# Kernel optimization log

Hardware: AMD Instinct MI355X
Metric: run time of the kernel (lower is better)

Reference implementation:

```python
import jax, jax.numpy as jnp
import numpy as np

EPS = 1e-6


def smooth(p):
    # smooth_distribution: clamp Bernoulli params away from {0,1}
    return jnp.clip(p, EPS, 1.0 - EPS)


def bern_logprob(p, x):
    # Bernoulli(p).log_prob(x) = x*log(p) + (1-x)*log(1-p)
    return x * jnp.log(p) + (1.0 - x) * jnp.log1p(-p)


def binary_row_reduce(A, b, k):
    # GF(2) Gaussian elimination on [A | b]; A:(k,n) binary float, b:(k,)
    M = jnp.concatenate([A, b[:, None]], axis=1)  # (k, n+1)
    rows = jnp.arange(k)
    for i in range(k):  # k is a small static int (25)
        col = M[:, i]
        cand = jnp.where((rows >= i) & (col > 0.5), rows, k)
        p = jnp.minimum(jnp.min(cand), k - 1)  # pivot row (fallback k-1 if none; prob ~0 for random A)
        ri, rp = M[i], M[p]
        M = M.at[i].set(rp)
        M = M.at[p].set(ri)
        elim = (M[:, i] > 0.5) & (rows != i)
        M = jnp.where(elim[:, None], jnp.mod(M + M[i], 2.0), M)
    return M[:, :-1], M[:, -1]


def compute_term1(logq, logp):
    # stable [sum_s q*log p]/[sum_s q], summed over batch; logq,logp: (S,B)
    m = jnp.max(logq, axis=0)                                  # (B,)
    w = jnp.exp(logq - m)                                      # (S,B)
    neg_num = m + jnp.log(jnp.sum(w * (-logp), axis=0))
    pos_den = m + jnp.log(jnp.sum(w, axis=0))
    return -jnp.sum(jnp.exp(neg_num - pos_den))


def setup_inputs() -> dict:
    key = jax.random.key(0)
    ks = jax.random.split(key, 5)
    nx, nz, B = 2048, 256, 512
    wr = float(np.sqrt(6.0 / (nx + nz)))
    xr = float(np.sqrt(6.0 / nx))
    zr = float(np.sqrt(6.0 / nz))
    U = jax.random.uniform(ks[0], (nz, nx), minval=-wr, maxval=wr)
    V = jax.random.uniform(ks[1], (nx, nz), minval=-wr, maxval=wr)
    x_bias = jax.random.uniform(ks[2], (nx,), minval=-xr, maxval=xr)
    z_bias = jax.random.uniform(ks[3], (nz,), minval=-zr, maxval=zr)
    xin = (jax.random.uniform(ks[4], (B, nx)) < 0.5).astype(jnp.float32)
    return {"xin": xin, "U": U, "V": V, "x_bias": x_bias, "z_bias": z_bias,
            "S": 10, "k": 25, "T": 30}


def reference(xin, U, V, x_bias, z_bias, S, k, T):
    dt = xin.dtype
    key = jax.random.key(42)
    kz, kx, kA, kb = jax.random.split(key, 4)

    # q(z|x) and samples  -------------------------------------------------
    q = smooth(jax.nn.sigmoid(xin @ U.T + z_bias))                     # (B, nz)
    samples_z = (jax.random.uniform(kz, (S,) + q.shape) < q).astype(dt)  # (S,B,nz)
    ps = smooth(jax.nn.sigmoid(jnp.einsum('sbz,xz->sbx', samples_z, V) + x_bias))  # (S,B,nx)
    xouts = (jax.random.uniform(kx, ps.shape) < ps).astype(dt)

    # projected ELBO over T random GF(2) hash constraints ------------------
    nz = U.shape[0]
    A_all = (jax.random.uniform(kA, (T, k, nz)) < 0.5).astype(dt)
    b_all = (jax.random.uniform(kb, (T, k)) < 0.5).astype(dt)
    pz = smooth(jax.nn.sigmoid(z_bias))                                # (nz,)

    def elbo_t(carry, Ab):
        A, b = Ab
        C, bp = binary_row_reduce(A, b, k)                             # (k,nz),(k,)
        proj = jnp.mod(jnp.einsum('sbz,kz->sbk', samples_z[:, :, k:], C[:, k:]) + bp, 2.0)
        sz = samples_z.at[:, :, :k].set(proj)                          # (S,B,nz)
        logq_zi = bern_logprob(q, sz).sum(axis=2)                      # (S,B)
        logp_z = bern_logprob(pz, sz).sum(axis=2)                      # (S,B)
        ps_t = smooth(jax.nn.sigmoid(jnp.einsum('sbz,xz->sbx', sz, V) + x_bias))
        logp_x = bern_logprob(ps_t, xin).sum(axis=2)                   # (S,B)
        logp = logp_z + logp_x
        term2 = compute_term1(logq_zi, logq_zi)
        term1 = compute_term1(logq_zi, logp)
        return carry, term1 - term2

    _, pelbos = jax.lax.scan(elbo_t, 0.0, (A_all, b_all))
    loss = -jnp.mean(pelbos)
    return q, samples_z, ps, xouts, loss
```

## Files before the change

### kernel.cpp

```cpp
#include <hip/hip_runtime.h>
#include <cstdint>

#define NX 2048
#define NZ 256
#define NB 512
#define NS 10
#define NK 25
#define NT 30
#define SBTOT (NS * NB)

#define LOG2E 1.4426950408889634f
#define LN2 0.6931471805599453f

#define OFF_Q 0
#define OFF_SAMP (NB * NZ)
#define OFF_PS (OFF_SAMP + SBTOT * NZ)
#define OFF_XO (OFF_PS + SBTOT * NX)
#define OFF_LOSS (OFF_XO + SBTOT * NX)

typedef unsigned long long ull;
typedef __bf16 bf16x8 __attribute__((ext_vector_type(8)));
typedef float f32x4 __attribute__((ext_vector_type(4)));

__host__ __device__ inline void tf2x32(uint32_t k0, uint32_t k1, uint32_t x0, uint32_t x1,
                                       uint32_t& o0, uint32_t& o1) {
  uint32_t k2 = k0 ^ k1 ^ 0x1BD11BDAu;
  x0 += k0; x1 += k1;
#define TF_R(r) { x0 += x1; x1 = (x1 << (r)) | (x1 >> (32 - (r))); x1 ^= x0; }
  TF_R(13) TF_R(15) TF_R(26) TF_R(6)
  x0 += k1; x1 += k2 + 1u;
  TF_R(17) TF_R(29) TF_R(16) TF_R(24)
  x0 += k2; x1 += k0 + 2u;
  TF_R(13) TF_R(15) TF_R(26) TF_R(6)
  x0 += k0; x1 += k1 + 3u;
  TF_R(17) TF_R(29) TF_R(16) TF_R(24)
  x0 += k1; x1 += k2 + 4u;
  TF_R(13) TF_R(15) TF_R(26) TF_R(6)
  x0 += k2; x1 += k0 + 5u;
#undef TF_R
  o0 = x0; o1 = x1;
}

__device__ inline uint32_t tf_select(uint32_t k0, uint32_t k1, uint32_t i, uint32_t h) {
  bool lo = i < h;
  uint32_t x0 = lo ? i : i - h;
  uint32_t x1 = lo ? i + h : i;
  uint32_t o0, o1;
  tf2x32(k0, k1, x0, x1, o0, o1);
  return lo ? o0 : o1;
}

__device__ inline float tf_uniform(uint32_t k0, uint32_t k1, uint32_t i, uint32_t h) {
  uint32_t r = tf_select(k0, k1, i, h);
  return __uint_as_float(0x3f800000u | (r >> 9)) - 1.0f;
}

__device__ inline float sigclip(float a) {
  float p = 1.0f / (1.0f + __expf(-a));
  return fminf(fmaxf(p, 1e-6f), 1.0f - 1e-6f);
}

__device__ inline ushort f2bf(float f) {
  uint32_t u = __float_as_uint(f);
  return (ushort)((u + 0x7FFFu + ((u >> 16) & 1u)) >> 16);
}

__device__ inline float blockReduceSum256(float v, volatile float* s4) {
#pragma unroll
  for (int o = 32; o > 0; o >>= 1) v += __shfl_down(v, o);
  __syncthreads();
  if ((threadIdx.x & 63) == 0) s4[threadIdx.x >> 6] = v;
  __syncthreads();
  return s4[0] + s4[1] + s4[2] + s4[3];
}

__global__ __launch_bounds__(256) void kP0_prep(const float* __restrict__ V,
                                                const float* __restrict__ U,
                                                const float* __restrict__ xin,
                                                const float* __restrict__ z_bias,
                                                ushort* __restrict__ Vbf,
                                                ushort* __restrict__ Vkpad2,
                                                ushort* __restrict__ Uhi,
                                                ushort* __restrict__ Ulo,
                                                ushort* __restrict__ xinbf,
                                                float* __restrict__ baseq,
                                                float* __restrict__ d_lpz,
                                                float* __restrict__ basepz) {
  __shared__ float red[4];
  int e = blockIdx.x * 256 + threadIdx.x;
  {
    int x = e >> 8, k = e & 255;
    float v = V[e];
    Vbf[e] = f2bf(v);
    if (k < 32) Vkpad2[x * 32 + k] = (k < NK) ? f2bf(v * LOG2E) : (ushort)0;
  }
  {
    float u = U[e];
    ushort hi = f2bf(u);
    Uhi[e] = hi;
    float hv = __uint_as_float((uint32_t)hi << 16);
    Ulo[e] = f2bf(u - hv);
  }
  {
    xinbf[e] = (xin[e] > 0.5f) ? (ushort)0x3F80 : (ushort)0;
    int e2 = e + NX * NZ;
    xinbf[e2] = (xin[e2] > 0.5f) ? (ushort)0x3F80 : (ushort)0;
  }
  if (e < NB) baseq[e] = 0.0f;
  if (blockIdx.x == 0) {
    int z = threadIdx.x;
    float pz = sigclip(z_bias[z]);
    float lp = __logf(pz), l1 = __logf(1.0f - pz);
    d_lpz[z] = lp - l1;
    float s = blockReduceSum256(l1, red);
    if (z == 0) *basepz = s;
  }
}

__global__ __launch_bounds__(256) void kW_signdot(const float* __restrict__ xin,
                                                  const ushort* __restrict__ Vkpad2,
                                                  float* __restrict__ W) {
  __shared__ float wred[4][NK];
  int b = blockIdx.x;
  int tid = threadIdx.x;
  float acc[NK];
#pragma unroll
  for (int j = 0; j < NK; ++j) acc[j] = 0.0f;
#pragma unroll
  for (int i = 0; i < 8; ++i) {
    int x = i * 256 + tid;
    float s = 1.0f - 2.0f * xin[(size_t)b * NX + x];
    const uint4* vp = (const uint4*)(Vkpad2 + (size_t)x * 32);
    uint4 q0 = vp[0], q1 = vp[1], q2 = vp[2], q3 = vp[3];
    uint32_t w[16] = {q0.x, q0.y, q0.z, q0.w, q1.x, q1.y, q1.z, q1.w,
                      q2.x, q2.y, q2.z, q2.w, q3.x, q3.y, q3.z, q3.w};
#pragma unroll
    for (int j = 0; j < NK; ++j) {
      uint32_t wd = w[j >> 1];
      float v = __uint_as_float((j & 1) ? (wd & 0xFFFF0000u) : (wd << 16));
      acc[j] = fmaf(s, v, acc[j]);
    }
  }
#pragma unroll
  for (int j = 0; j < NK; ++j) {
#pragma unroll
    for (int o = 1; o < 64; o <<= 1) acc[j] += __shfl_xor(acc[j], o);
  }
  if ((tid & 63) == 0) {
#pragma unroll
    for (int j = 0; j < NK; ++j) wred[tid >> 6][j] = acc[j];
  }
  __syncthreads();
  if (tid < NK) W[b * 32 + tid] = wred[0][tid] + wred[1][tid] + wred[2][tid] + wred[3][tid];
}

__global__ __launch_bounds__(256) void k1a_mfma(const ushort* __restrict__ xinbf,
                                                const ushort* __restrict__ Uhi,
                                                const ushort* __restrict__ Ulo,
                                                const float* __restrict__ z_bias,
                                                float* __restrict__ outq,
                                                float* __restrict__ d_lq,
                                                float* __restrict__ baseq) {
  __shared__ float red[4][16][17];
  int tid = threadIdx.x;
  int wave = tid >> 6, lane = tid & 63, grp = lane >> 4, col = lane & 15;
  int b0 = (blockIdx.x >> 4) * 16;
  int z0 = (blockIdx.x & 15) * 16;
  f32x4 acc = {0.f, 0.f, 0.f, 0.f};
  const ushort* arow = xinbf + (size_t)(b0 + col) * NX + wave * 512 + grp * 8;
  const ushort* bhr = Uhi + (size_t)(z0 + col) * NX + wave * 512 + grp * 8;
  const ushort* blr = Ulo + (size_t)(z0 + col) * NX + wave * 512 + grp * 8;
#pragma unroll 4
  for (int s = 0; s < 16; ++s) {
    bf16x8 a = *(const bf16x8*)(arow + s * 32);
    bf16x8 bh = *(const bf16x8*)(bhr + s * 32);
    bf16x8 bl = *(const bf16x8*)(blr + s * 32);
    acc = __builtin_amdgcn_mfma_f32_16x16x32_bf16(a, bh, acc, 0, 0, 0);
    acc = __builtin_amdgcn_mfma_f32_16x16x32_bf16(a, bl, acc, 0, 0, 0);
  }
#pragma unroll
  for (int r = 0; r < 4; ++r) red[wave][grp * 4 + r][col] = acc[r];
  __syncthreads();
  int bi = tid >> 4, zi = tid & 15;
  float aa = red[0][bi][zi] + red[1][bi][zi] + red[2][bi][zi] + red[3][bi][zi] + z_bias[z0 + zi];
  int b = b0 + bi, z = z0 + zi;
  float q = sigclip(aa);
  outq[b * NZ + z] = q;
  float lq = __logf(q), l1 = __logf(1.0f - q);
  d_lq[b * NZ + z] = lq - l1;
  float s1 = l1;
#pragma unroll
  for (int o = 1; o < 16; o <<= 1) s1 += __shfl_xor(s1, o);
  if (zi == 0) atomicAdd(&baseq[b], s1);
}

__global__ __launch_bounds__(256) void k2_samples(const float* __restrict__ q,
                                                  const float* __restrict__ d_lq,
                                                  const float* __restrict__ d_lpz,
                                                  const ull* __restrict__ Ct,
                                                  const uint32_t* __restrict__ bpmask,
                                                  const float* __restrict__ W,
                                                  float* __restrict__ samp_out,
                                                  ushort* __restrict__ samp16,
                                                  ull* __restrict__ Spack,
                                                  float* __restrict__ qtail,
                                                  float* __restrict__ ptail,
                                                  uint32_t* __restrict__ projb,
                                                  float* __restrict__ Syd,
                                                  uint32_t kz0, uint32_t kz1) {
  __shared__ float red[4];
  __shared__ ull sp_sh[4];
  int sb = blockIdx.x;
  int z = threadIdx.x;
  int b = sb & (NB - 1);
  uint32_t i = (uint32_t)sb * NZ + z;
  const uint32_t h = (uint32_t)SBTOT * NZ / 2;
  float u = tf_uniform(kz0, kz1, i, h);
  float qv = q[b * NZ + z];
  int smp = (u < qv) ? 1 : 0;
  samp_out[i] = (float)smp;
  samp16[i] = smp ? (ushort)0x3F80 : (ushort)0;
  ull m = __ballot(smp);
  if ((z & 63) == 0) { Spack[sb * 4 + (z >> 6)] = m; sp_sh[z >> 6] = m; }
  float dq = (z >= NK && smp) ? d_lq[b * NZ + z] : 0.0f;
  float dp = (z >= NK && smp) ? d_lpz[z] : 0.0f;
  float sq = blockReduceSum256(dq, red);
  float sp = blockReduceSum256(dp, red);
  if (z == 0) { qtail[sb] = sq; ptail[sb] = sp; }
  if (z < 32) {
    int t = z;
    ull s0 = sp_sh[0], s1 = sp_sh[1], s2 = sp_sh[2], s3 = sp_sh[3];
    uint32_t s25 = (uint32_t)(s0 & 0x1FFFFFFull);
    const float* Wb = W + (size_t)b * 32;
    uint32_t out;
    float syd = 0.0f;
    if (t < NT) {
      uint32_t bp = bpmask[t];
      uint32_t pb = 0;
#pragma unroll
      for (int j = 0; j < NK; ++j) {
        const ull* C = Ct + (size_t)(t * NK + j) * 4;
        int par = __popcll(s0 & C[0]) + __popcll(s1 & C[1]) + __popcll(s2 & C[2]) + __popcll(s3 & C[3]);
        uint32_t bit = ((uint32_t)(par ^ (int)(bp >> j))) & 1u;
        pb |= bit << j;
        int d = (int)bit - (int)((s25 >> j) & 1u);
        syd = fmaf((float)d, Wb[j], syd);
      }
      out = pb;
    } else {
      out = s25;
    }
    projb[sb * 32 + t] = out;
    Syd[sb * 32 + t] = syd;
  }
}

__global__ __launch_bounds__(256) void k3m_gemm(const ushort* __restrict__ samp16,
                                                const ushort* __restrict__ Vbf,
                                                const float* __restrict__ x_bias,
                                                ushort* __restrict__ base2,
                                                float* __restrict__ ps_out,
                                                float* __restrict__ xo_out,
                                                uint32_t kx0, uint32_t kx1) {
  __shared__ __align__(16) char smem[2 * 2112 * 4];
  ushort* As = (ushort*)smem;
  ushort* Bs = (ushort*)(smem + 8192);
  float* Tt = (float*)smem;

  int tid = threadIdx.x;
  int wave = tid >> 6, lane = tid & 63, grp = lane >> 4, col = lane & 15;
  int x0 = blockIdx.x * 128;
  int sb0 = blockIdx.y * 32;
  f32x4 acc[2][4];
#pragma unroll
  for (int mi = 0; mi < 2; ++mi)
#pragma unroll
    for (int ni = 0; ni < 4; ++ni) acc[mi][ni] = (f32x4){0.f, 0.f, 0.f, 0.f};

  for (int k0 = 0; k0 < NZ; k0 += 32) {
    {
      int rowb = tid >> 2, kcb = (tid & 3) << 3;
      int sbrow = (rowb < 32) ? (sb0 + rowb) : (sb0 + 2528 + rowb);
      *(uint4*)&Bs[rowb * 32 + kcb] = *(const uint4*)&samp16[(size_t)sbrow * NZ + k0 + kcb];
#pragma unroll
      for (int c = tid; c < 512; c += 256) {
        int rowa = c >> 2, kca = (c & 3) << 3;
        *(uint4*)&As[rowa * 32 + kca] = *(const uint4*)&Vbf[(size_t)(x0 + rowa) * NZ + k0 + kca];
      }
    }
    __syncthreads();
    bf16x8 af[2], bfv[4];
#pragma unroll
    for (int mi = 0; mi < 2; ++mi)
      af[mi] = *(const bf16x8*)&As[(wave * 32 + mi * 16 + col) * 32 + grp * 8];
#pragma unroll
    for (int ni = 0; ni < 4; ++ni)
      bfv[ni] = *(const bf16x8*)&Bs[(ni * 16 + col) * 32 + grp * 8];
#pragma unroll
    for (int mi = 0; mi < 2; ++mi)
#pragma unroll
      for (int ni = 0; ni < 4; ++ni)
        acc[mi][ni] = __builtin_amdgcn_mfma_f32_16x16x32_bf16(af[mi], bfv[ni], acc[mi][ni], 0, 0, 0);
    __syncthreads();
  }

  const uint32_t HH = (uint32_t)(SBTOT / 2) * (uint32_t)NX;
#pragma unroll
  for (int pi = 0; pi < 2; ++pi) {
    __syncthreads();
#pragma unroll
    for (int mi = 0; mi < 2; ++mi) {
      int cbase = wave * 32 + mi * 16 + grp * 4;
      *(float4*)&Tt[col * 132 + cbase] = *(float4*)&acc[mi][pi];
      *(float4*)&Tt[2112 + col * 132 + cbase] = *(float4*)&acc[mi][pi + 2];
    }
    __syncthreads();
#pragma unroll
    for (int pass = 0; pass < 2; ++pass) {
      int r = pass * 8 + (tid >> 5);
      int c = (tid & 31) * 4;
      float4 t0 = *(float4*)&Tt[r * 132 + c];
      float4 t1 = *(float4*)&Tt[2112 + r * 132 + c];
      float4 xb4 = *(const float4*)(x_bias + x0 + c);
      int sb_a = sb0 + pi * 16 + r;
      size_t off_a = (size_t)sb_a * NX + x0 + c;
      size_t off_b = off_a + (size_t)HH;
      float a0 = t0.x + xb4.x, a1 = t0.y + xb4.y, a2 = t0.z + xb4.z, a3 = t0.w + xb4.w;
      float b0 = t1.x + xb4.x, b1 = t1.y + xb4.y, b2 = t1.z + xb4.z, b3 = t1.w + xb4.w;
      uint2 bpa, bpb;
      bpa.x = (uint32_t)f2bf(a0 * LOG2E) | ((uint32_t)f2bf(a1 * LOG2E) << 16);
      bpa.y = (uint32_t)f2bf(a2 * LOG2E) | ((uint32_t)f2bf(a3 * LOG2E) << 16);
      bpb.x = (uint32_t)f2bf(b0 * LOG2E) | ((uint32_t)f2bf(b1 * LOG2E) << 16);
      bpb.y = (uint32_t)f2bf(b2 * LOG2E) | ((uint32_t)f2bf(b3 * LOG2E) << 16);
      *(uint2*)(base2 + off_a) = bpa;
      *(uint2*)(base2 + off_b) = bpb;
      float4 pva = make_float4(sigclip(a0), sigclip(a1), sigclip(a2), sigclip(a3));
      float4 pvb = make_float4(sigclip(b0), sigclip(b1), sigclip(b2), sigclip(b3));
      *(float4*)(ps_out + off_a) = pva;
      *(float4*)(ps_out + off_b) = pvb;
      uint32_t fi = (uint32_t)off_a;
      uint32_t r0, r1;
      float4 xva, xvb;
      tf2x32(kx0, kx1, fi + 0u, fi + 0u + HH, r0, r1);
      xva.x = ((__uint_as_float(0x3f800000u | (r0 >> 9)) - 1.0f) < pva.x) ? 1.0f : 0.0f;
      xvb.x = ((__uint_as_float(0x3f800000u | (r1 >> 9)) - 1.0f) < pvb.x) ? 1.0f : 0.0f;
      tf2x32(kx0, kx1, fi + 1u, fi + 1u + HH, r0, r1);
      xva.y = ((__uint_as_float(0x3f800000u | (r0 >> 9)) - 1.0f) < pva.y) ? 1.0f : 0.0f;
      xvb.y = ((__uint_as_float(0x3f800000u | (r1 >> 9)) - 1.0f) < pvb.y) ? 1.0f : 0.0f;
      tf2x32(kx0, kx1, fi + 2u, fi + 2u + HH, r0, r1);
      xva.z = ((__uint_as_float(0x3f800000u | (r0 >> 9)) - 1.0f) < pva.z) ? 1.0f : 0.0f;
      xvb.z = ((__uint_as_float(0x3f800000u | (r1 >> 9)) - 1.0f) < pvb.z) ? 1.0f : 0.0f;
      tf2x32(kx0, kx1, fi + 3u, fi + 3u + HH, r0, r1);
      xva.w = ((__uint_as_float(0x3f800000u | (r0 >> 9)) - 1.0f) < pva.w) ? 1.0f : 0.0f;
      xvb.w = ((__uint_as_float(0x3f800000u | (r1 >> 9)) - 1.0f) < pvb.w) ? 1.0f : 0.0f;
      *(float4*)(xo_out + off_a) = xva;
      *(float4*)(xo_out + off_b) = xvb;
    }
  }
}

__global__ __launch_bounds__(256) void k4_rowreduce(ull* __restrict__ Ct,
                                                    uint32_t* __restrict__ bpmask,
                                                    uint32_t kA0, uint32_t kA1,
                                                    uint32_t kb0, uint32_t kb1) {
  __shared__ uint32_t Aw[NK][8];
  __shared__ uint32_t bbsh[NK];
  int t = blockIdx.x;
  int tid = threadIdx.x;
  if (tid < NK * 8) {
    int r = tid >> 3, c = tid & 7;
    const uint32_t hA = (uint32_t)NT * NK * NZ / 2;
    uint32_t base_i = (uint32_t)(t * NK + r) * NZ + c * 32;
    uint32_t w = 0;
    for (int zz = 0; zz < 32; ++zz) {
      uint32_t rr = tf_select(kA0, kA1, base_i + zz, hA);
      w |= ((rr >> 31) ^ 1u) << zz;
    }
    Aw[r][c] = w;
  }
  if (tid < NK) {
    const uint32_t hb = (uint32_t)NT * NK / 2;
    uint32_t rb = tf_select(kb0, kb1, (uint32_t)(t * NK + tid), hb);
    bbsh[tid] = (rb >> 31) ^ 1u;
  }
  __syncthreads();
  if (tid >= 64) return;
  int lane = tid;
  ull w0 = 0, w1 = 0, w2 = 0, w3 = 0;
  uint32_t bbit = 0;
  if (lane < NK) {
    w0 = (ull)Aw[lane][0] | ((ull)Aw[lane][1] << 32);
    w1 = (ull)Aw[lane][2] | ((ull)Aw[lane][3] << 32);
    w2 = (ull)Aw[lane][4] | ((ull)Aw[lane][5] << 32);
    w3 = (ull)Aw[lane][6] | ((ull)Aw[lane][7] << 32);
    bbit = bbsh[lane];
  }
  for (int i = 0; i < NK; ++i) {
    int mybit = (int)((w0 >> i) & 1ull);
    ull mask = __ballot(lane < NK && mybit);
    ull cand = mask & (~0ull << i);
    int p = cand ? __builtin_ctzll(cand) : (NK - 1);
    int srcl = (lane == i) ? p : ((lane == p) ? i : lane);
    w0 = __shfl(w0, srcl); w1 = __shfl(w1, srcl); w2 = __shfl(w2, srcl); w3 = __shfl(w3, srcl);
    bbit = __shfl(bbit, srcl);
    ull p0 = __shfl(w0, i), p1 = __shfl(w1, i), p2 = __shfl(w2, i), p3 = __shfl(w3, i);
    uint32_t pvb = __shfl(bbit, i);
    int nb2 = (int)((w0 >> i) & 1ull);
    if (lane < NK && lane != i && nb2) {
      w0 ^= p0; w1 ^= p1; w2 ^= p2; w3 ^= p3; bbit ^= pvb;
    }
  }
  if (lane < NK) {
    w0 &= ~((1ull << NK) - 1ull);
    ull* dstp = Ct + (size_t)(t * NK + lane) * 4;
    dstp[0] = w0; dstp[1] = w1; dstp[2] = w2; dstp[3] = w3;
  }
  ull bm = __ballot(lane < NK && bbit);
  if (lane == 0) bpmask[t] = (uint32_t)bm & 0x1FFFFFFu;
}

__global__ __launch_bounds__(256) void k6_mfma(const ushort* __restrict__ base2,
                                               const ushort* __restrict__ Vkpad2,
                                               const float* __restrict__ xin,
                                               const uint32_t* __restrict__ projb,
                                               const ull* __restrict__ Spack,
                                               const float* __restrict__ Syd,
                                               float* __restrict__ logpx) {
  __shared__ float bvsm[NX];
  __shared__ float lsum[4][32];
  __shared__ float red[4];
  int sb = blockIdx.x;
  int b = sb & (NB - 1);
  int tid = threadIdx.x;
  int wave = tid >> 6, lane = tid & 63;
  int grp = lane >> 4, col = lane & 15;
  const uint4* b16p = (const uint4*)(base2 + (size_t)sb * NX);
  const float4* x4p = (const float4*)(xin + (size_t)b * NX);
  float sbacc = 0.0f;
  {
    uint4 bu = b16p[tid];
    float4 xv0 = x4p[tid * 2], xv1 = x4p[tid * 2 + 1];
    uint32_t wds[4] = {bu.x, bu.y, bu.z, bu.w};
    float bv[8];
#pragma unroll
    for (int j = 0; j < 8; ++j) {
      uint32_t wd = wds[j >> 1];
      bv[j] = __uint_as_float((j & 1) ? (wd & 0xFFFF0000u) : (wd << 16));
    }
    float sg[8] = {1.0f - 2.0f * xv0.x, 1.0f - 2.0f * xv0.y, 1.0f - 2.0f * xv0.z,
                   1.0f - 2.0f * xv0.w, 1.0f - 2.0f * xv1.x, 1.0f - 2.0f * xv1.y,
                   1.0f - 2.0f * xv1.z, 1.0f - 2.0f * xv1.w};
#pragma unroll
    for (int j = 0; j < 8; ++j) {
      bvsm[tid * 8 + j] = bv[j];
      sbacc = fmaf(sg[j], bv[j], sbacc);
    }
  }
  float Sb = blockReduceSum256(sbacc, red);
  uint32_t s25 = (uint32_t)(Spack[sb * 4] & 0x1FFFFFFull);
  uint32_t pb0 = projb[sb * 32 + col];
  uint32_t pb1 = projb[sb * 32 + 16 + col];
  bf16x8 a0, a1;
  union { ushort u; __bf16 hh; } cvt;
#pragma unroll
  for (int j = 0; j < 8; ++j) {
    int k = grp * 8 + j;
    int sbit = (int)((s25 >> k) & 1u);
    int d0 = (int)((pb0 >> k) & 1u) - sbit;
    int d1 = (int)((pb1 >> k) & 1u) - sbit;
    cvt.u = (ushort)(d0 == 0 ? 0 : (d0 > 0 ? 0x3F80 : 0xBF80)); a0[j] = cvt.hh;
    cvt.u = (ushort)(d1 == 0 ? 0 : (d1 > 0 ? 0x3F80 : 0xBF80)); a1[j] = cvt.hh;
  }
  float acca[8], pp[8];
#pragma unroll
  for (int r = 0; r < 8; ++r) { acca[r] = 0.0f; pp[r] = 1.0f; }
  const ushort* vkp = Vkpad2 + (size_t)(wave * 512 + col) * 32 + grp * 8;
  const float* bvp = bvsm + wave * 512 + col;
  bf16x8 bcur = *(const bf16x8*)(vkp);
#pragma unroll 8
  for (int i = 0; i < 32; ++i) {
    bf16x8 bnxt = bcur;
    if (i < 31) bnxt = *(const bf16x8*)(vkp + (size_t)(i + 1) * 512);
    f32x4 c0 = {0.f, 0.f, 0.f, 0.f}, c1 = {0.f, 0.f, 0.f, 0.f};
    c0 = __builtin_amdgcn_mfma_f32_16x16x32_bf16(a0, bcur, c0, 0, 0, 0);
    c1 = __builtin_amdgcn_mfma_f32_16x16x32_bf16(a1, bcur, c1, 0, 0, 0);
    float bs = bvp[i * 16];
#pragma unroll
    for (int r = 0; r < 4; ++r) {
      float y0 = bs + c0[r];
      acca[r] += fabsf(y0);
      pp[r] = fmaf(pp[r], __builtin_amdgcn_exp2f(-fabsf(y0)), pp[r]);
      float y1 = bs + c1[r];
      acca[4 + r] += fabsf(y1);
      pp[4 + r] = fmaf(pp[4 + r], __builtin_amdgcn_exp2f(-fabsf(y1)), pp[4 + r]);
    }
    bcur = bnxt;
  }
#pragma unroll
  for (int r = 0; r < 8; ++r) {
    float m = 0.5f * acca[r] + __log2f(pp[r]);
#pragma unroll
    for (int off = 1; off < 16; off <<= 1) m += __shfl_xor(m, off);
    if (col == 0) {
      int t = (r < 4) ? (grp * 4 + r) : (16 + grp * 4 + (r - 4));
      lsum[wave][t] = m;
    }
  }
  __syncthreads();
  if (tid < NT) {
    float tot = lsum[0][tid] + lsum[1][tid] + lsum[2][tid] + lsum[3][tid];
    tot += 0.5f * (Sb + Syd[sb * 32 + tid]);
    logpx[(size_t)tid * SBTOT + sb] = -LN2 * tot;
  }
}

__global__ __launch_bounds__(64) void k7_reduce(const float* __restrict__ logpx,
                                                const uint32_t* __restrict__ projb,
                                                const float* __restrict__ qtail,
                                                const float* __restrict__ ptail,
                                                const float* __restrict__ baseq,
                                                const float* __restrict__ d_lq,
                                                const float* __restrict__ d_lpz,
                                                const float* __restrict__ basepz,
                                                double* __restrict__ pelbo_part) {
  int t = blockIdx.x;
  int chunk = blockIdx.y;
  int lane = threadIdx.x;
  int b = chunk * 64 + lane;
  float dlq[NK];
#pragma unroll
  for (int j = 0; j < NK; ++j) dlq[j] = d_lq[b * NZ + j];
  float bq = baseq[b];
  float bpz = *basepz;
  float lq[NS], lp[NS];
#pragma unroll
  for (int s = 0; s < NS; ++s) {
    int sb = s * NB + b;
    uint32_t m = projb[sb * 32 + t];
    float sq = 0.0f, spv = 0.0f;
#pragma unroll
    for (int j = 0; j < NK; ++j) {
      float on = (float)((m >> j) & 1u);
      sq += on * dlq[j];
      spv += on * d_lpz[j];
    }
    lq[s] = bq + qtail[sb] + sq;
    lp[s] = logpx[t * SBTOT + sb] + bpz + ptail[sb] + spv;
  }
  float mx = lq[0];
#pragma unroll
  for (int s = 1; s < NS; ++s) mx = fmaxf(mx, lq[s]);
  float den = 0.0f, num = 0.0f;
#pragma unroll
  for (int s = 0; s < NS; ++s) {
    float w = __expf(lq[s] - mx);
    den += w;
    num += w * (lq[s] - lp[s]);
  }
  double v = (double)(num / den);
#pragma unroll
  for (int o = 32; o > 0; o >>= 1) v += __shfl_down(v, o);
  if (lane == 0) pelbo_part[t * 8 + chunk] = v;
}

__global__ __launch_bounds__(64) void k8_loss(const double* __restrict__ pelbo_part,
                                              float* __restrict__ out_loss) {
  int t = threadIdx.x;
  double v = 0.0;
  if (t < NT) {
#pragma unroll
    for (int c = 0; c < 8; ++c) v += pelbo_part[t * 8 + c];
  }
#pragma unroll
  for (int o = 32; o > 0; o >>= 1) v += __shfl_down(v, o);
  if (t == 0) *out_loss = (float)(v / (double)NT);
}

extern "C" void kernel_launch(void* const* d_in, const int* in_sizes, int n_in,
                              void* d_out, int out_size, void* d_ws, size_t ws_size,
                              hipStream_t stream) {
  const float* xin = (const float*)d_in[0];
  const float* U = (const float*)d_in[1];
  const float* V = (const float*)d_in[2];
  const float* x_bias = (const float*)d_in[3];
  const float* z_bias = (const float*)d_in[4];
  float* out = (float*)d_out;

  char* p = (char*)d_ws;
  ushort* base2 = (ushort*)p;             p += (size_t)SBTOT * NX * 2;
  float* d_lq = (float*)p;                p += (size_t)NB * NZ * 4;
  float* baseq = (float*)p;               p += (size_t)NB * 4;
  float* d_lpz = (float*)p;               p += (size_t)NZ * 4;
  float* basepz = (float*)p;              p += 16;
  ull* Spack = (ull*)p;                   p += (size_t)SBTOT * 4 * 8;
  float* qtail = (float*)p;               p += (size_t)SBTOT * 4;
  float* ptail = (float*)p;               p += (size_t)SBTOT * 4;
  ull* Ct = (ull*)p;                      p += (size_t)NT * NK * 4 * 8;
  uint32_t* bpm = (uint32_t*)p;           p += 128;
  uint32_t* projb = (uint32_t*)p;         p += (size_t)SBTOT * 32 * 4;
  float* Syd = (float*)p;                 p += (size_t)SBTOT * 32 * 4;
  float* logpx = (float*)p;               p += (size_t)NT * SBTOT * 4;
  double* pelbo = (double*)p;             p += (size_t)NT * 8 * 8;
  ushort* Vkpad2 = (ushort*)p;            p += (size_t)NX * 32 * 2;
  ushort* Vbf = (ushort*)p;               p += (size_t)NX * NZ * 2;
  ushort* samp16 = (ushort*)p;            p += (size_t)SBTOT * NZ * 2;
  float* W = (float*)p;                   p += (size_t)NB * 32 * 4;
  ushort* Uhi = (ushort*)p;               p += (size_t)NZ * NX * 2;
  ushort* Ulo = (ushort*)p;               p += (size_t)NZ * NX * 2;
  ushort* xinbf = (ushort*)p;             p += (size_t)NB * NX * 2;
  (void)ws_size; (void)in_sizes; (void)n_in; (void)out_size;

  uint32_t o0[4], o1[4];
  for (int j = 0; j < 4; ++j) tf2x32(0u, 42u, (uint32_t)j, (uint32_t)(4 + j), o0[j], o1[j]);
  uint32_t kz0 = o0[0], kz1 = o0[1];
  uint32_t kx0 = o0[2], kx1 = o0[3];
  uint32_t kA0 = o1[0], kA1 = o1[1];
  uint32_t kb0 = o1[2], kb1 = o1[3];

  kP0_prep<<<NX * NZ / 256, 256, 0, stream>>>(V, U, xin, z_bias, Vbf, Vkpad2,
                                              Uhi, Ulo, xinbf, baseq, d_lpz, basepz);
  k4_rowreduce<<<NT, 256, 0, stream>>>(Ct, bpm, kA0, kA1, kb0, kb1);
  k1a_mfma<<<512, 256, 0, stream>>>(xinbf, Uhi, Ulo, z_bias, out + OFF_Q, d_lq, baseq);
  kW_signdot<<<NB, 256, 0, stream>>>(xin, Vkpad2, W);
  k2_samples<<<SBTOT, 256, 0, stream>>>(out + OFF_Q, d_lq, d_lpz, Ct, bpm, W,
                                        out + OFF_SAMP, samp16, Spack, qtail, ptail,
                                        projb, Syd, kz0, kz1);
  dim3 g3(NX / 128, SBTOT / 64);
  k3m_gemm<<<g3, 256, 0, stream>>>(samp16, Vbf, x_bias, base2,
                                   out + OFF_PS, out + OFF_XO, kx0, kx1);
  k6_mfma<<<SBTOT, 256, 0, stream>>>(base2, Vkpad2, xin, projb, Spack, Syd, logpx);
  dim3 g7(NT, 8);
  k7_reduce<<<g7, 64, 0, stream>>>(logpx, projb, qtail, ptail, baseq, d_lq,
                                   d_lpz, basepz, pelbo);
  k8_loss<<<1, 64, 0, stream>>>(pelbo, out + OFF_LOSS);
}
```

Baseline: 270.0 us.

## Merge small independent kernels into shared launches and simplify k6 B-fragment loads

The GF(2) row-reduce blocks now run as extra blocks appended to the prep kernel, and the q-GEMM and the W sign-dot are merged into one 1024-block launch, which cuts the launch count from four to two. The aim is to remove per-launch overhead and the idle tail of the small kernels. In k6 the software-prefetched double buffer for the V fragment is replaced by direct loads with unroll 4, with the index recomputed per iteration. This lowers register pressure but may expose load latency. The merged launches also raise LDS use per block, since each now declares the shared arrays of both branches.

```diff
diff --git a/kernel.cpp b/kernel.cpp
--- a/kernel.cpp
+++ b/kernel.cpp
@@ -85,9 +85,70 @@
                                                 ushort* __restrict__ xinbf,
                                                 float* __restrict__ baseq,
                                                 float* __restrict__ d_lpz,
-                                                float* __restrict__ basepz) {
+                                                float* __restrict__ basepz,
+                                                ull* __restrict__ Ct,
+                                                uint32_t* __restrict__ bpmask,
+                                                uint32_t kA0, uint32_t kA1,
+                                                uint32_t kb0, uint32_t kb1) {
   __shared__ float red[4];
-  int e = blockIdx.x * 256 + threadIdx.x;
+  __shared__ uint32_t Aw[NK][8];
+  __shared__ uint32_t bbsh[NK];
+  int tid = threadIdx.x;
+  if (blockIdx.x >= NX * NZ / 256) {
+    int t = blockIdx.x - NX * NZ / 256;
+    if (tid < NK * 8) {
+      int r = tid >> 3, c = tid & 7;
+      const uint32_t hA = (uint32_t)NT * NK * NZ / 2;
+      uint32_t base_i = (uint32_t)(t * NK + r) * NZ + c * 32;
+      uint32_t w = 0;
+      for (int zz = 0; zz < 32; ++zz) {
+        uint32_t rr = tf_select(kA0, kA1, base_i + zz, hA);
+        w |= ((rr >> 31) ^ 1u) << zz;
+      }
+      Aw[r][c] = w;
+    }
+    if (tid < NK) {
+      const uint32_t hb = (uint32_t)NT * NK / 2;
+      uint32_t rb = tf_select(kb0, kb1, (uint32_t)(t * NK + tid), hb);
+      bbsh[tid] = (rb >> 31) ^ 1u;
+    }
+    __syncthreads();
+    if (tid >= 64) return;
+    int lane = tid;
+    ull w0 = 0, w1 = 0, w2 = 0, w3 = 0;
+    uint32_t bbit = 0;
+    if (lane < NK) {
+      w0 = (ull)Aw[lane][0] | ((ull)Aw[lane][1] << 32);
+      w1 = (ull)Aw[lane][2] | ((ull)Aw[lane][3] << 32);
+      w2 = (ull)Aw[lane][4] | ((ull)Aw[lane][5] << 32);
+      w3 = (ull)Aw[lane][6] | ((ull)Aw[lane][7] << 32);
+      bbit = bbsh[lane];
+    }
+    for (int i = 0; i < NK; ++i) {
+      int mybit = (int)((w0 >> i) & 1ull);
+      ull mask = __ballot(lane < NK && mybit);
+      ull cand = mask & (~0ull << i);
+      int p = cand ? __builtin_ctzll(cand) : (NK - 1);
+      int srcl = (lane == i) ? p : ((lane == p) ? i : lane);
+      w0 = __shfl(w0, srcl); w1 = __shfl(w1, srcl); w2 = __shfl(w2, srcl); w3 = __shfl(w3, srcl);
+      bbit = __shfl(bbit, srcl);
+      ull p0 = __shfl(w0, i), p1 = __shfl(w1, i), p2 = __shfl(w2, i), p3 = __shfl(w3, i);
+      uint32_t pvb = __shfl(bbit, i);
+      int nb2 = (int)((w0 >> i) & 1ull);
+      if (lane < NK && lane != i && nb2) {
+        w0 ^= p0; w1 ^= p1; w2 ^= p2; w3 ^= p3; bbit ^= pvb;
+      }
+    }
+    if (lane < NK) {
+      w0 &= ~((1ull << NK) - 1ull);
+      ull* dstp = Ct + (size_t)(t * NK + lane) * 4;
+      dstp[0] = w0; dstp[1] = w1; dstp[2] = w2; dstp[3] = w3;
+    }
+    ull bm = __ballot(lane < NK && bbit);
+    if (lane == 0) bpmask[t] = (uint32_t)bm & 0x1FFFFFFu;
+    return;
+  }
+  int e = blockIdx.x * 256 + tid;
   {
     int x = e >> 8, k = e & 255;
     float v = V[e];
@@ -108,7 +169,7 @@
   }
   if (e < NB) baseq[e] = 0.0f;
   if (blockIdx.x == 0) {
-    int z = threadIdx.x;
+    int z = tid;
     float pz = sigclip(z_bias[z]);
     float lp = __logf(pz), l1 = __logf(1.0f - pz);
     d_lpz[z] = lp - l1;
@@ -117,12 +178,52 @@
   }
 }
 
-__global__ __launch_bounds__(256) void kW_signdot(const float* __restrict__ xin,
-                                                  const ushort* __restrict__ Vkpad2,
-                                                  float* __restrict__ W) {
+__global__ __launch_bounds__(256) void k1w_mfma(const ushort* __restrict__ xinbf,
+                                                const ushort* __restrict__ Uhi,
+                                                const ushort* __restrict__ Ulo,
+                                                const float* __restrict__ z_bias,
+                                                const float* __restrict__ xin,
+                                                const ushort* __restrict__ Vkpad2,
+                                                float* __restrict__ outq,
+                                                float* __restrict__ d_lq,
+                                                float* __restrict__ baseq,
+                                                float* __restrict__ W) {
+  __shared__ float red[4][16][17];
   __shared__ float wred[4][NK];
-  int b = blockIdx.x;
   int tid = threadIdx.x;
+  if (blockIdx.x < 512) {
+    int wave = tid >> 6, lane = tid & 63, grp = lane >> 4, col = lane & 15;
+    int b0 = (blockIdx.x >> 4) * 16;
+    int z0 = (blockIdx.x & 15) * 16;
+    f32x4 acc = {0.f, 0.f, 0.f, 0.f};
+    const ushort* arow = xinbf + (size_t)(b0 + col) * NX + wave * 512 + grp * 8;
+    const ushort* bhr = Uhi + (size_t)(z0 + col) * NX + wave * 512 + grp * 8;
+    const ushort* blr = Ulo + (size_t)(z0 + col) * NX + wave * 512 + grp * 8;
+#pragma unroll 4
+    for (int s = 0; s < 16; ++s) {
+      bf16x8 a = *(const bf16x8*)(arow + s * 32);
+      bf16x8 bh = *(const bf16x8*)(bhr + s * 32);
+      bf16x8 bl = *(const bf16x8*)(blr + s * 32);
+      acc = __builtin_amdgcn_mfma_f32_16x16x32_bf16(a, bh, acc, 0, 0, 0);
+      acc = __builtin_amdgcn_mfma_f32_16x16x32_bf16(a, bl, acc, 0, 0, 0);
+    }
+#pragma unroll
+    for (int r = 0; r < 4; ++r) red[wave][grp * 4 + r][col] = acc[r];
+    __syncthreads();
+    int bi = tid >> 4, zi = tid & 15;
+    float aa = red[0][bi][zi] + red[1][bi][zi] + red[2][bi][zi] + red[3][bi][zi] + z_bias[z0 + zi];
+    int b = b0 + bi, z = z0 + zi;
+    float q = sigclip(aa);
+    outq[b * NZ + z] = q;
+    float lq = __logf(q), l1 = __logf(1.0f - q);
+    d_lq[b * NZ + z] = lq - l1;
+    float s1 = l1;
+#pragma unroll
+    for (int o = 1; o < 16; o <<= 1) s1 += __shfl_xor(s1, o);
+    if (zi == 0) atomicAdd(&baseq[b], s1);
+    return;
+  }
+  int b = blockIdx.x - 512;
   float acc[NK];
 #pragma unroll
   for (int j = 0; j < NK; ++j) acc[j] = 0.0f;
@@ -152,46 +253,6 @@
   }
   __syncthreads();
   if (tid < NK) W[b * 32 + tid] = wred[0][tid] + wred[1][tid] + wred[2][tid] + wred[3][tid];
-}
-
-__global__ __launch_bounds__(256) void k1a_mfma(const ushort* __restrict__ xinbf,
-                                                const ushort* __restrict__ Uhi,
-                                                const ushort* __restrict__ Ulo,
-                                                const float* __restrict__ z_bias,
-                                                float* __restrict__ outq,
-                                                float* __restrict__ d_lq,
-                                                float* __restrict__ baseq) {
-  __shared__ float red[4][16][17];
-  int tid = threadIdx.x;
-  int wave = tid >> 6, lane = tid & 63, grp = lane >> 4, col = lane & 15;
-  int b0 = (blockIdx.x >> 4) * 16;
-  int z0 = (blockIdx.x & 15) * 16;
-  f32x4 acc = {0.f, 0.f, 0.f, 0.f};
-  const ushort* arow = xinbf + (size_t)(b0 + col) * NX + wave * 512 + grp * 8;
-  const ushort* bhr = Uhi + (size_t)(z0 + col) * NX + wave * 512 + grp * 8;
-  const ushort* blr = Ulo + (size_t)(z0 + col) * NX + wave * 512 + grp * 8;
-#pragma unroll 4
-  for (int s = 0; s < 16; ++s) {
-    bf16x8 a = *(const bf16x8*)(arow + s * 32);
-    bf16x8 bh = *(const bf16x8*)(bhr + s * 32);
-    bf16x8 bl = *(const bf16x8*)(blr + s * 32);
-    acc = __builtin_amdgcn_mfma_f32_16x16x32_bf16(a, bh, acc, 0, 0, 0);
-    acc = __builtin_amdgcn_mfma_f32_16x16x32_bf16(a, bl, acc, 0, 0, 0);
-  }
-#pragma unroll
-  for (int r = 0; r < 4; ++r) red[wave][grp * 4 + r][col] = acc[r];
-  __syncthreads();
-  int bi = tid >> 4, zi = tid & 15;
-  float aa = red[0][bi][zi] + red[1][bi][zi] + red[2][bi][zi] + red[3][bi][zi] + z_bias[z0 + zi];
-  int b = b0 + bi, z = z0 + zi;
-  float q = sigclip(aa);
-  outq[b * NZ + z] = q;
-  float lq = __logf(q), l1 = __logf(1.0f - q);
-  d_lq[b * NZ + z] = lq - l1;
-  float s1 = l1;
-#pragma unroll
-  for (int o = 1; o < 16; o <<= 1) s1 += __shfl_xor(s1, o);
-  if (zi == 0) atomicAdd(&baseq[b], s1);
 }
 
 __global__ __launch_bounds__(256) void k2_samples(const float* __restrict__ q,
@@ -359,66 +420,6 @@
   }
 }
 
-__global__ __launch_bounds__(256) void k4_rowreduce(ull* __restrict__ Ct,
-                                                    uint32_t* __restrict__ bpmask,
-                                                    uint32_t kA0, uint32_t kA1,
-                                                    uint32_t kb0, uint32_t kb1) {
-  __shared__ uint32_t Aw[NK][8];
-  __shared__ uint32_t bbsh[NK];
-  int t = blockIdx.x;
-  int tid = threadIdx.x;
-  if (tid < NK * 8) {
-    int r = tid >> 3, c = tid & 7;
-    const uint32_t hA = (uint32_t)NT * NK * NZ / 2;
-    uint32_t base_i = (uint32_t)(t * NK + r) * NZ + c * 32;
-    uint32_t w = 0;
-    for (int zz = 0; zz < 32; ++zz) {
-      uint32_t rr = tf_select(kA0, kA1, base_i + zz, hA);
-      w |= ((rr >> 31) ^ 1u) << zz;
-    }
-    Aw[r][c] = w;
-  }
-  if (tid < NK) {
-    const uint32_t hb = (uint32_t)NT * NK / 2;
-    uint32_t rb = tf_select(kb0, kb1, (uint32_t)(t * NK + tid), hb);
-    bbsh[tid] = (rb >> 31) ^ 1u;
-  }
-  __syncthreads();
-  if (tid >= 64) return;
-  int lane = tid;
-  ull w0 = 0, w1 = 0, w2 = 0, w3 = 0;
-  uint32_t bbit = 0;
-  if (lane < NK) {
-    w0 = (ull)Aw[lane][0] | ((ull)Aw[lane][1] << 32);
-    w1 = (ull)Aw[lane][2] | ((ull)Aw[lane][3] << 32);
-    w2 = (ull)Aw[lane][4] | ((ull)Aw[lane][5] << 32);
-    w3 = (ull)Aw[lane][6] | ((ull)Aw[lane][7] << 32);
-    bbit = bbsh[lane];
-  }
-  for (int i = 0; i < NK; ++i) {
-    int mybit = (int)((w0 >> i) & 1ull);
-    ull mask = __ballot(lane < NK && mybit);
-    ull cand = mask & (~0ull << i);
-    int p = cand ? __builtin_ctzll(cand) : (NK - 1);
-    int srcl = (lane == i) ? p : ((lane == p) ? i : lane);
-    w0 = __shfl(w0, srcl); w1 = __shfl(w1, srcl); w2 = __shfl(w2, srcl); w3 = __shfl(w3, srcl);
-    bbit = __shfl(bbit, srcl);
-    ull p0 = __shfl(w0, i), p1 = __shfl(w1, i), p2 = __shfl(w2, i), p3 = __shfl(w3, i);
-    uint32_t pvb = __shfl(bbit, i);
-    int nb2 = (int)((w0 >> i) & 1ull);
-    if (lane < NK && lane != i && nb2) {
-      w0 ^= p0; w1 ^= p1; w2 ^= p2; w3 ^= p3; bbit ^= pvb;
-    }
-  }
-  if (lane < NK) {
-    w0 &= ~((1ull << NK) - 1ull);
-    ull* dstp = Ct + (size_t)(t * NK + lane) * 4;
-    dstp[0] = w0; dstp[1] = w1; dstp[2] = w2; dstp[3] = w3;
-  }
-  ull bm = __ballot(lane < NK && bbit);
-  if (lane == 0) bpmask[t] = (uint32_t)bm & 0x1FFFFFFu;
-}
-
 __global__ __launch_bounds__(256) void k6_mfma(const ushort* __restrict__ base2,
                                                const ushort* __restrict__ Vkpad2,
                                                const float* __restrict__ xin,
@@ -474,17 +475,15 @@
   float acca[8], pp[8];
 #pragma unroll
   for (int r = 0; r < 8; ++r) { acca[r] = 0.0f; pp[r] = 1.0f; }
-  const ushort* vkp = Vkpad2 + (size_t)(wave * 512 + col) * 32 + grp * 8;
-  const float* bvp = bvsm + wave * 512 + col;
-  bf16x8 bcur = *(const bf16x8*)(vkp);
-#pragma unroll 8
+  const ushort* vkbase = Vkpad2 + (size_t)(wave * 512 + col) * 32 + grp * 8;
+#pragma unroll 4
   for (int i = 0; i < 32; ++i) {
-    bf16x8 bnxt = bcur;
-    if (i < 31) bnxt = *(const bf16x8*)(vkp + (size_t)(i + 1) * 512);
+    int x = (wave * 32 + i) * 16 + col;
+    bf16x8 bfr = *(const bf16x8*)(vkbase + (size_t)i * 16 * 32);
     f32x4 c0 = {0.f, 0.f, 0.f, 0.f}, c1 = {0.f, 0.f, 0.f, 0.f};
-    c0 = __builtin_amdgcn_mfma_f32_16x16x32_bf16(a0, bcur, c0, 0, 0, 0);
-    c1 = __builtin_amdgcn_mfma_f32_16x16x32_bf16(a1, bcur, c1, 0, 0, 0);
-    float bs = bvp[i * 16];
+    c0 = __builtin_amdgcn_mfma_f32_16x16x32_bf16(a0, bfr, c0, 0, 0, 0);
+    c1 = __builtin_amdgcn_mfma_f32_16x16x32_bf16(a1, bfr, c1, 0, 0, 0);
+    float bs = bvsm[x];
 #pragma unroll
     for (int r = 0; r < 4; ++r) {
       float y0 = bs + c0[r];
@@ -494,7 +493,6 @@
       acca[4 + r] += fabsf(y1);
       pp[4 + r] = fmaf(pp[4 + r], __builtin_amdgcn_exp2f(-fabsf(y1)), pp[4 + r]);
     }
-    bcur = bnxt;
   }
 #pragma unroll
   for (int r = 0; r < 8; ++r) {
@@ -617,11 +615,11 @@
   uint32_t kA0 = o1[0], kA1 = o1[1];
   uint32_t kb0 = o1[2], kb1 = o1[3];
 
-  kP0_prep<<<NX * NZ / 256, 256, 0, stream>>>(V, U, xin, z_bias, Vbf, Vkpad2,
-                                              Uhi, Ulo, xinbf, baseq, d_lpz, basepz);
-  k4_rowreduce<<<NT, 256, 0, stream>>>(Ct, bpm, kA0, kA1, kb0, kb1);
-  k1a_mfma<<<512, 256, 0, stream>>>(xinbf, Uhi, Ulo, z_bias, out + OFF_Q, d_lq, baseq);
-  kW_signdot<<<NB, 256, 0, stream>>>(xin, Vkpad2, W);
+  kP0_prep<<<NX * NZ / 256 + NT, 256, 0, stream>>>(V, U, xin, z_bias, Vbf, Vkpad2,
+                                                   Uhi, Ulo, xinbf, baseq, d_lpz, basepz,
+                                                   Ct, bpm, kA0, kA1, kb0, kb1);
+  k1w_mfma<<<1024, 256, 0, stream>>>(xinbf, Uhi, Ulo, z_bias, xin, Vkpad2,
+                                     out + OFF_Q, d_lq, baseq, W);
   k2_samples<<<SBTOT, 256, 0, stream>>>(out + OFF_Q, d_lq, d_lpz, Ct, bpm, W,
                                         out + OFF_SAMP, samp16, Spack, qtail, ptail,
                                         projb, Syd, kz0, kz1);
```

After: 258.1 us. 4.4% less time.
